# Kernel optimization log

Measured on AMD Instinct MI355X. Metric: run time of the kernel, lower is better.

Reference implementation:

```python
import jax, jax.numpy as jnp
import numpy as np

N = 500_000      # active input voxels
C = 64           # feature channels
B = 2            # batch size
RES = 256        # input spatial resolution (coords in [0, RES))
FACTOR = 2       # downsample factor (init kwarg)


def setup_inputs() -> dict:
    key = jax.random.key(0)
    k1, k2, k3 = jax.random.split(key, 3)
    feats = jax.random.normal(k1, (N, C), dtype=jnp.float32)
    bidx = jax.random.randint(k2, (N, 1), 0, B, dtype=jnp.int32)
    xyz = jax.random.randint(k3, (N, 3), 0, RES, dtype=jnp.int32)
    coords = jnp.concatenate([bidx, xyz], axis=1)  # [N, 4] = (b, x, y, z)
    return {"feats": feats, "coords": coords}


def reference(feats, coords):
    """Sparse voxel downsample: coord hashing + dedup + scatter-mean pooling.

    Returns (new_feats [N, C], new_coords [N, 4]); rows beyond the number of
    unique downsampled voxels are zero-feature / coord = -1 padding (JAX needs
    static shapes; torch original returns only the n_unique valid rows).
    """
    res = RES // FACTOR  # static spatial extent after downsampling
    b = coords[:, 0].astype(jnp.int32)
    xyz = coords[:, 1:] // FACTOR  # [N, 3]
    # linear hash code = ((b*res + x)*res + y)*res + z
    code = ((b * res + xyz[:, 0]) * res + xyz[:, 1]) * res + xyz[:, 2]
    uniq, inv = jnp.unique(code, size=N, fill_value=-1, return_inverse=True)
    # mean pooling with include_self=False == segment_sum / segment_count
    counts = jax.ops.segment_sum(jnp.ones((N,), feats.dtype), inv, num_segments=N)
    sums = jax.ops.segment_sum(feats, inv, num_segments=N)  # [N, C]
    new_feats = sums / jnp.maximum(counts, 1.0)[:, None]
    # decode unique codes back to (b, x, y, z)
    valid = counts > 0
    z = uniq % res
    y = (uniq // res) % res
    x = (uniq // (res * res)) % res
    nb = uniq // (res * res * res)
    new_coords = jnp.stack([nb, x, y, z], axis=-1).astype(jnp.int32)
    new_coords = jnp.where(valid[:, None], new_coords, -1)
    return new_feats, new_coords
```

## Files before the change

kernel.cpp:

```cpp
#include <hip/hip_runtime.h>


#define RES2 128
#define NCODES (2 * 128 * 128 * 128)
#define NW (NCODES / 4)
#define HBLK 4096

typedef unsigned long long u64;
typedef float f4 __attribute__((ext_vector_type(4)));

__global__ void count_codes(const int* __restrict__ coords,
                            unsigned* __restrict__ cnt8,
                            int* __restrict__ codes, int n) {
    int i = blockIdx.x * 256 + threadIdx.x;
    if (i >= n) return;
    const int4 v = reinterpret_cast<const int4*>(coords)[i];
    int code = (((v.x * RES2 + (v.y >> 1)) * RES2 + (v.z >> 1)) * RES2) + (v.w >> 1);
    codes[i] = code;
    atomicAdd(&cnt8[code >> 2], 1u << (8 * (code & 3)));
}

__global__ void block_sums(const unsigned* __restrict__ cnt8,
                           u64* __restrict__ btot) {
    __shared__ u64 sh[256];
    int t = threadIdx.x;
    unsigned w = cnt8[blockIdx.x * 256 + t];
    unsigned c0 = w & 0xFFu, c1 = (w >> 8) & 0xFFu,
             c2 = (w >> 16) & 0xFFu, c3 = w >> 24;
    u64 s = ((u64)(c0 + c1 + c2 + c3) << 32) |
            (u64)((c0 != 0) + (c1 != 0) + (c2 != 0) + (c3 != 0));
    sh[t] = s;
    __syncthreads();
    for (int off = 128; off > 0; off >>= 1) {
        if (t < off) sh[t] += sh[t + off];
        __syncthreads();
    }
    if (t == 0) btot[blockIdx.x] = sh[0];
}

__global__ void scan_totals(u64* __restrict__ btot, unsigned* __restrict__ nuq) {
    __shared__ u64 sh[1024];
    int t = threadIdx.x;
    int base = t * 4;
    u64 v[4], e[4], s = 0;
#pragma unroll
    for (int j = 0; j < 4; ++j) { v[j] = btot[base + j]; e[j] = s; s += v[j]; }
    sh[t] = s;
    __syncthreads();
    for (int off = 1; off < 1024; off <<= 1) {
        u64 add = (t >= off) ? sh[t - off] : 0ull;
        __syncthreads();
        sh[t] += add;
        __syncthreads();
    }
    u64 excl = (t == 0) ? 0ull : sh[t - 1];
#pragma unroll
    for (int j = 0; j < 4; ++j) btot[base + j] = excl + e[j];
    if (t == 1023) *nuq = (unsigned)(sh[1023] & 0xFFFFFFFFull);
}

__global__ void scan_write(const unsigned* __restrict__ cnt8,
                           const u64* __restrict__ btot,
                           unsigned* __restrict__ rank_tab,
                           unsigned* __restrict__ uniq_cc,
                           unsigned* __restrict__ row_end) {
    __shared__ u64 sh[256];
    int t = threadIdx.x;
    unsigned w = cnt8[blockIdx.x * 256 + t];
    unsigned c4[4] = {w & 0xFFu, (w >> 8) & 0xFFu, (w >> 16) & 0xFFu, w >> 24};
    u64 e[4], s = 0;
#pragma unroll
    for (int j = 0; j < 4; ++j) {
        e[j] = s;
        s += ((u64)c4[j] << 32) | (u64)(c4[j] != 0);
    }
    sh[t] = s;
    __syncthreads();
    for (int off = 1; off < 256; off <<= 1) {
        u64 add = (t >= off) ? sh[t - off] : 0ull;
        __syncthreads();
        sh[t] += add;
        __syncthreads();
    }
    u64 texcl = ((t == 0) ? 0ull : sh[t - 1]) + btot[blockIdx.x];
    int cbase = (blockIdx.x * 256 + t) * 4;
#pragma unroll
    for (int j = 0; j < 4; ++j) {
        if (c4[j]) {
            unsigned r = (unsigned)((texcl + e[j]) & 0xFFFFFFFFull);
            unsigned st = (unsigned)((texcl + e[j]) >> 32);
            int code = cbase + j;
            rank_tab[code] = r;
            uniq_cc[r] = (unsigned)code | (c4[j] << 22);
            row_end[r] = st;
        }
    }
}

__global__ void fill_sorted(const int* __restrict__ codes,
                            const unsigned* __restrict__ rank_tab,
                            unsigned* __restrict__ row_end,
                            int* __restrict__ sorted_idx, int n) {
    int i = blockIdx.x * 256 + threadIdx.x;
    if (i >= n) return;
    unsigned r = rank_tab[codes[i]];
    unsigned pos = atomicAdd(&row_end[r], 1u);
    sorted_idx[pos] = i;
}

__global__ void gather32(const f4* __restrict__ feats4,
                         const int* __restrict__ sorted_idx,
                         const unsigned* __restrict__ row_end,
                         const unsigned* __restrict__ uniq_cc,
                         const unsigned* __restrict__ nuq_p,
                         f4* __restrict__ outF4,
                         f4* __restrict__ outC4, int n) {
    int tid = blockIdx.x * 256 + threadIdx.x;
    int wave = tid >> 6;
    int lane = threadIdx.x & 63;
    int q = lane >> 4;
    int sub = lane & 15;
    int rb = wave * 32 + q;
    int nuq = (int)*nuq_p;

    if (rb + 28 < nuq) {
        int r[8];
        unsigned en[8], cc[8];
#pragma unroll
        for (int k = 0; k < 8; ++k) r[k] = rb + k * 4;
#pragma unroll
        for (int k = 0; k < 8; ++k) en[k] = row_end[r[k]];
#pragma unroll
        for (int k = 0; k < 8; ++k) cc[k] = uniq_cc[r[k]];
        int cnt[8], st[8], i0[8];
#pragma unroll
        for (int k = 0; k < 8; ++k) {
            cnt[k] = (int)(cc[k] >> 22);
            st[k] = (int)en[k] - cnt[k];
        }
#pragma unroll
        for (int k = 0; k < 8; ++k) i0[k] = sorted_idx[st[k]];
        f4 a[8];
#pragma unroll
        for (int k = 0; k < 8; ++k)
            a[k] = __builtin_nontemporal_load(&feats4[(size_t)i0[k] * 16 + sub]);
#pragma unroll
        for (int k = 0; k < 8; ++k) {
            if (cnt[k] > 1) {
                for (int m = 1; m < cnt[k]; ++m) {
                    int i = sorted_idx[st[k] + m];
                    f4 v = __builtin_nontemporal_load(&feats4[(size_t)i * 16 + sub]);
                    a[k] += v;
                }
                a[k] *= (1.0f / (float)cnt[k]);
            }
            __builtin_nontemporal_store(a[k], &outF4[(size_t)r[k] * 16 + sub]);
            if (sub == 0) {
                unsigned code = cc[k] & 0x3FFFFFu;
                f4 cv = {(float)(code >> 21), (float)((code >> 14) & 127),
                         (float)((code >> 7) & 127), (float)(code & 127)};
                __builtin_nontemporal_store(cv, &outC4[r[k]]);
            }
        }
    } else {
#pragma unroll
        for (int k = 0; k < 8; ++k) {
            int r = rb + k * 4;
            if (r >= n) continue;
            if (r < nuq) {
                unsigned en = row_end[r];
                unsigned cc = uniq_cc[r];
                int cnt = (int)(cc >> 22);
                int st = (int)en - cnt;
                f4 a = {0.f, 0.f, 0.f, 0.f};
                for (int m = 0; m < cnt; ++m) {
                    int i = sorted_idx[st + m];
                    a += feats4[(size_t)i * 16 + sub];
                }
                a *= (1.0f / (float)cnt);
                outF4[(size_t)r * 16 + sub] = a;
                if (sub == 0) {
                    unsigned code = cc & 0x3FFFFFu;
                    f4 cv = {(float)(code >> 21), (float)((code >> 14) & 127),
                             (float)((code >> 7) & 127), (float)(code & 127)};
                    outC4[r] = cv;
                }
            } else {
                f4 zz = {0.f, 0.f, 0.f, 0.f};
                outF4[(size_t)r * 16 + sub] = zz;
                if (sub == 0) {
                    f4 mm = {-1.f, -1.f, -1.f, -1.f};
                    outC4[r] = mm;
                }
            }
        }
    }
}

extern "C" void kernel_launch(void* const* d_in, const int* in_sizes, int n_in,
                              void* d_out, int out_size, void* d_ws, size_t ws_size,
                              hipStream_t stream) {
    const float* feats = (const float*)d_in[0];
    const int* coords = (const int*)d_in[1];
    const int n = in_sizes[1] / 4;

    float* outF = (float*)d_out;
    f4* outC4 = (f4*)(outF + (size_t)n * 64);

    unsigned* cnt8 = (unsigned*)d_ws;
    u64* btot = (u64*)(cnt8 + NW);
    unsigned* nuq = (unsigned*)(btot + HBLK);
    int* codes = (int*)(nuq + 2);
    unsigned* rank_tab = (unsigned*)(codes + n);
    unsigned* uniq_cc = rank_tab + NCODES;
    unsigned* row_end = uniq_cc + n;
    int* sorted_idx = (int*)(row_end + n);

    (void)hipMemsetAsync(cnt8, 0, (size_t)NW * sizeof(unsigned), stream);

    count_codes<<<(n + 255) / 256, 256, 0, stream>>>(coords, cnt8, codes, n);
    block_sums<<<HBLK, 256, 0, stream>>>(cnt8, btot);
    scan_totals<<<1, 1024, 0, stream>>>(btot, nuq);
    scan_write<<<HBLK, 256, 0, stream>>>(cnt8, btot, rank_tab, uniq_cc, row_end);
    fill_sorted<<<(n + 255) / 256, 256, 0, stream>>>(codes, rank_tab, row_end, sorted_idx, n);

    int waves = (n + 31) / 32;
    int blocks = (waves * 64 + 255) / 256;
    gather32<<<blocks, 256, 0, stream>>>((const f4*)feats, sorted_idx,
                                         row_end, uniq_cc, nuq,
                                         (f4*)outF, outC4, n);
}
```

Measured before the change: 130.9 us.

## Replace per-code rank table with per-word prefix and drop nontemporal loads

Instead of scattering a rank for every occupied code into a large per-code rank table, scan_write now stores one 32-bit unique-prefix per 4-code word. fill_sorted rebuilds the rank from that prefix plus the occupancy of the earlier bytes in the packed count word. This replaces scattered writes into the per-code table with a dense, coalesced write of a quarter-size table, at the cost of one extra read per element in fill_sorted. Separately, the gather kernel switches feature loads from nontemporal to ordinary cached loads.

```diff
diff --git a/kernel.cpp b/kernel.cpp
--- a/kernel.cpp
+++ b/kernel.cpp
@@ -61,12 +61,13 @@
 
 __global__ void scan_write(const unsigned* __restrict__ cnt8,
                            const u64* __restrict__ btot,
-                           unsigned* __restrict__ rank_tab,
+                           unsigned* __restrict__ wprefix,
                            unsigned* __restrict__ uniq_cc,
                            unsigned* __restrict__ row_end) {
     __shared__ u64 sh[256];
     int t = threadIdx.x;
-    unsigned w = cnt8[blockIdx.x * 256 + t];
+    int widx = blockIdx.x * 256 + t;
+    unsigned w = cnt8[widx];
     unsigned c4[4] = {w & 0xFFu, (w >> 8) & 0xFFu, (w >> 16) & 0xFFu, w >> 24};
     u64 e[4], s = 0;
 #pragma unroll
@@ -83,14 +84,14 @@
         __syncthreads();
     }
     u64 texcl = ((t == 0) ? 0ull : sh[t - 1]) + btot[blockIdx.x];
-    int cbase = (blockIdx.x * 256 + t) * 4;
+    wprefix[widx] = (unsigned)(texcl & 0xFFFFFFFFull);
+    int cbase = widx * 4;
 #pragma unroll
     for (int j = 0; j < 4; ++j) {
         if (c4[j]) {
             unsigned r = (unsigned)((texcl + e[j]) & 0xFFFFFFFFull);
             unsigned st = (unsigned)((texcl + e[j]) >> 32);
             int code = cbase + j;
-            rank_tab[code] = r;
             uniq_cc[r] = (unsigned)code | (c4[j] << 22);
             row_end[r] = st;
         }
@@ -98,12 +99,21 @@
 }
 
 __global__ void fill_sorted(const int* __restrict__ codes,
-                            const unsigned* __restrict__ rank_tab,
+                            const unsigned* __restrict__ cnt8,
+                            const unsigned* __restrict__ wprefix,
                             unsigned* __restrict__ row_end,
                             int* __restrict__ sorted_idx, int n) {
     int i = blockIdx.x * 256 + threadIdx.x;
     if (i >= n) return;
-    unsigned r = rank_tab[codes[i]];
+    int c = codes[i];
+    unsigned w = cnt8[c >> 2];
+    unsigned base = wprefix[c >> 2];
+    int j = c & 3;
+    unsigned occ = 0;
+    if (j > 0) occ += ((w & 0xFFu) != 0);
+    if (j > 1) occ += (((w >> 8) & 0xFFu) != 0);
+    if (j > 2) occ += (((w >> 16) & 0xFFu) != 0);
+    unsigned r = base + occ;
     unsigned pos = atomicAdd(&row_end[r], 1u);
     sorted_idx[pos] = i;
 }
@@ -143,14 +153,13 @@
         f4 a[8];
 #pragma unroll
         for (int k = 0; k < 8; ++k)
-            a[k] = __builtin_nontemporal_load(&feats4[(size_t)i0[k] * 16 + sub]);
+            a[k] = feats4[(size_t)i0[k] * 16 + sub];
 #pragma unroll
         for (int k = 0; k < 8; ++k) {
             if (cnt[k] > 1) {
                 for (int m = 1; m < cnt[k]; ++m) {
                     int i = sorted_idx[st[k] + m];
-                    f4 v = __builtin_nontemporal_load(&feats4[(size_t)i * 16 + sub]);
-                    a[k] += v;
+                    a[k] += feats4[(size_t)i * 16 + sub];
                 }
                 a[k] *= (1.0f / (float)cnt[k]);
             }
@@ -211,8 +220,8 @@
     u64* btot = (u64*)(cnt8 + NW);
     unsigned* nuq = (unsigned*)(btot + HBLK);
     int* codes = (int*)(nuq + 2);
-    unsigned* rank_tab = (unsigned*)(codes + n);
-    unsigned* uniq_cc = rank_tab + NCODES;
+    unsigned* wprefix = (unsigned*)(codes + n);
+    unsigned* uniq_cc = wprefix + NW;
     unsigned* row_end = uniq_cc + n;
     int* sorted_idx = (int*)(row_end + n);
 
@@ -221,8 +230,8 @@
     count_codes<<<(n + 255) / 256, 256, 0, stream>>>(coords, cnt8, codes, n);
     block_sums<<<HBLK, 256, 0, stream>>>(cnt8, btot);
     scan_totals<<<1, 1024, 0, stream>>>(btot, nuq);
-    scan_write<<<HBLK, 256, 0, stream>>>(cnt8, btot, rank_tab, uniq_cc, row_end);
-    fill_sorted<<<(n + 255) / 256, 256, 0, stream>>>(codes, rank_tab, row_end, sorted_idx, n);
+    scan_write<<<HBLK, 256, 0, stream>>>(cnt8, btot, wprefix, uniq_cc, row_end);
+    fill_sorted<<<(n + 255) / 256, 256, 0, stream>>>(codes, cnt8, wprefix, row_end, sorted_idx, n);
 
     int waves = (n + 31) / 32;
     int blocks = (waves * 64 + 255) / 256;
```

Result: faster. 119.6 us (-8.6%).
